# Performance work log

Hardware: AMD Instinct MI355X
Metric: run time of the kernel (lower is better)

The kernel has to match this reference:

```python
import jax, jax.numpy as jnp
import numpy as np

POS_SCALE = 50.0
LEN_SCALE = 500.0

N_NODES = 100000
N_EDGES = 600000
IN_DIM = 128
HID_DIM = 128


def setup_inputs() -> dict:
    key = jax.random.key(0)
    ks = jax.random.split(key, 12)
    x = jax.random.normal(ks[0], (N_NODES, IN_DIM), dtype=jnp.float32)
    positions = jax.random.randint(ks[1], (N_NODES,), 0, 50, dtype=jnp.int64)
    lengths = jax.random.randint(ks[2], (N_NODES,), 0, 500, dtype=jnp.int64)
    edge_index = jax.random.randint(ks[3], (2, N_EDGES), 0, N_NODES, dtype=jnp.int64)
    reranker_scores = jax.random.normal(ks[4], (N_NODES,), dtype=jnp.float32)
    s = 1.0 / np.sqrt(IN_DIM + 2)
    fp_w = jax.random.uniform(ks[5], (IN_DIM + 2, IN_DIM), minval=-s, maxval=s, dtype=jnp.float32)
    fp_b = jnp.zeros((IN_DIM,), jnp.float32)
    s2 = 1.0 / np.sqrt(IN_DIM)
    lin_l_w = jax.random.uniform(ks[6], (IN_DIM, HID_DIM), minval=-s2, maxval=s2, dtype=jnp.float32)
    lin_l_b = jnp.zeros((HID_DIM,), jnp.float32)
    lin_r_w = jax.random.uniform(ks[7], (IN_DIM, HID_DIM), minval=-s2, maxval=s2, dtype=jnp.float32)
    res_w = jax.random.uniform(ks[8], (IN_DIM, HID_DIM), minval=-s2, maxval=s2, dtype=jnp.float32)
    res_b = jnp.zeros((HID_DIM,), jnp.float32)
    s3 = 1.0 / np.sqrt(HID_DIM)
    sh_w = jax.random.uniform(ks[9], (HID_DIM, 1), minval=-s3, maxval=s3, dtype=jnp.float32)
    sh_b = jnp.zeros((1,), jnp.float32)
    alpha = jnp.asarray(0.65, jnp.float32)
    return {
        "x": x, "positions": positions, "lengths": lengths,
        "edge_index": edge_index, "reranker_scores": reranker_scores,
        "fp_w": fp_w, "fp_b": fp_b,
        "lin_l_w": lin_l_w, "lin_l_b": lin_l_b, "lin_r_w": lin_r_w,
        "res_w": res_w, "res_b": res_b,
        "sh_w": sh_w, "sh_b": sh_b, "alpha": alpha,
    }


def reference(x, positions, lengths, edge_index, reranker_scores,
              fp_w, fp_b, lin_l_w, lin_l_b, lin_r_w, res_w, res_b,
              sh_w, sh_b, alpha):
    n = x.shape[0]
    # position/length features
    pos_feat = positions[:, None].astype(x.dtype) / POS_SCALE
    len_feat = lengths[:, None].astype(x.dtype) / LEN_SCALE
    xf = jnp.concatenate([x, pos_feat, len_feat], axis=-1)  # [N, D+2]
    xf = xf @ fp_w + fp_b                                   # [N, D]
    h_in = xf @ res_w + res_b                               # residual proj [N, H]
    # SAGEConv with mean aggregation: out = lin_l(mean_{j->i} x_j) + lin_r(x_i)
    src, dst = edge_index[0], edge_index[1]
    msg_sum = jax.ops.segment_sum(xf[src], dst, num_segments=n)          # [N, D]
    cnt = jax.ops.segment_sum(jnp.ones((src.shape[0], 1), xf.dtype), dst, num_segments=n)
    agg = msg_sum / jnp.maximum(cnt, 1.0)
    h = jax.nn.relu(agg @ lin_l_w + lin_l_b + xf @ lin_r_w)  # [N, H]
    # dropout is identity in eval mode
    h = h + h_in
    gnn_scores = (h @ sh_w + sh_b)[:, 0]                     # [N]
    a = jax.nn.sigmoid(alpha)
    return a * reranker_scores + (1.0 - a) * gnn_scores
```

## Files before the change

### kernel.cpp

```cpp
#include <hip/hip_runtime.h>
#include <hip/hip_bf16.h>
#include <cstdint>

#define D 128
#define LDSPITCH 136
#define CAP 32

typedef __attribute__((ext_vector_type(4))) float f32x4;
typedef __attribute__((ext_vector_type(2))) float f32x2;
typedef __attribute__((ext_vector_type(8))) short s16x8;

__device__ __forceinline__ unsigned short f2b(float f) {
    union { float f; uint32_t u; } v; v.f = f;
    uint32_t b = v.u + 0x7fffu + ((v.u >> 16) & 1u);
    return (unsigned short)(b >> 16);
}
__device__ __forceinline__ float b2f(unsigned short u) {
    union { uint32_t u; float f; } v; v.u = ((uint32_t)u) << 16; return v.f;
}

#if __has_builtin(__builtin_amdgcn_cvt_pk_fp8_f32) && __has_builtin(__builtin_amdgcn_cvt_pk_f32_fp8)
#define FP8_HW 1
__device__ __forceinline__ unsigned char f_to_fp8(float f) {
    int r = __builtin_amdgcn_cvt_pk_fp8_f32(f, 0.f, 0, false);
    return (unsigned char)(r & 0xff);
}
__device__ __forceinline__ void fp8x8_acc(float* t, int wx, int wy) {
    f32x2 p0 = __builtin_amdgcn_cvt_pk_f32_fp8(wx, false);
    f32x2 p1 = __builtin_amdgcn_cvt_pk_f32_fp8(wx, true);
    f32x2 p2 = __builtin_amdgcn_cvt_pk_f32_fp8(wy, false);
    f32x2 p3 = __builtin_amdgcn_cvt_pk_f32_fp8(wy, true);
    t[0] += p0.x; t[1] += p0.y; t[2] += p1.x; t[3] += p1.y;
    t[4] += p2.x; t[5] += p2.y; t[6] += p3.x; t[7] += p3.y;
}
#else
__device__ __forceinline__ unsigned char f_to_fp8(float f) {
    union { float f; uint32_t u; } v; v.f = f;
    uint32_t s = (v.u >> 31) << 7;
    uint32_t bits = v.u & 0x7fffffffu;
    if (bits < 0x3a800000u) return (unsigned char)s;
    uint32_t r = bits + 0x7ffffu + ((bits >> 20) & 1u);
    int ee = (int)(r >> 23) - 127 + 7;
    uint32_t man = (r >> 20) & 7u;
    if (ee <= 0) return (unsigned char)s;
    if (ee > 15) { ee = 15; man = 6; }
    if (ee == 15 && man == 7) man = 6;
    return (unsigned char)(s | ((uint32_t)ee << 3) | man);
}
__device__ __forceinline__ float fp8_one(unsigned char u) {
    int s = u >> 7, e = (u >> 3) & 15, m = u & 7;
    if (e == 0) { float v = (float)m * 0.001953125f; return s ? -v : v; }
    union { uint32_t u; float f; } w;
    w.u = ((uint32_t)s << 31) | ((uint32_t)(e + 120) << 23) | ((uint32_t)m << 20);
    return w.f;
}
__device__ __forceinline__ void fp8x8_acc(float* t, int wx, int wy) {
    uint32_t a = (uint32_t)wx, b = (uint32_t)wy;
#pragma unroll
    for (int k = 0; k < 4; ++k) t[k] += fp8_one((a >> (8 * k)) & 0xff);
#pragma unroll
    for (int k = 0; k < 4; ++k) t[4 + k] += fp8_one((b >> (8 * k)) & 0xff);
}
#endif

__global__ __launch_bounds__(256) void k_prep(
    const float* __restrict__ fp_w, const float* __restrict__ lin_l_w,
    const float* __restrict__ lin_r_w,
    unsigned short* __restrict__ Btf, unsigned short* __restrict__ Btl,
    unsigned short* __restrict__ Btr,
    const float* __restrict__ res_w, const float* __restrict__ res_b,
    const float* __restrict__ sh_w, const float* __restrict__ sh_b,
    const float* __restrict__ alpha, float* __restrict__ c1, float* __restrict__ scal,
    int* __restrict__ cursor, int* __restrict__ srcs,
    unsigned short* __restrict__ xb, unsigned char* __restrict__ xf8,
    int N, int zb) {
    int bid = blockIdx.x, tid = threadIdx.x;
    if (bid < 192) {
        int m = bid >> 6;
        int i = (bid & 63) * 256 + tid;
        const float* src = (m == 0) ? fp_w : (m == 1) ? lin_l_w : lin_r_w;
        unsigned short* dst = (m == 0) ? Btf : (m == 1) ? Btl : Btr;
        int k = i >> 7, n = i & 127;
        dst[n * D + k] = f2b(src[k * D + n]);
    } else if (bid == 192) {
        if (tid < 128) {
            float s = 0.f;
            for (int j = 0; j < D; ++j) s += res_w[tid * D + j] * sh_w[j];
            c1[tid] = s;
            if (tid == 0) {
                float c0 = 0.f;
                for (int j = 0; j < D; ++j) c0 += res_b[j] * sh_w[j];
                c0 += sh_b[0];
                float a = 1.f / (1.f + expf(-alpha[0]));
                scal[0] = a; scal[1] = c0;
            }
        } else if (tid < 192) {
            ((unsigned int*)(xb + (size_t)N * D))[tid - 128] = 0u;
        } else if (tid < 224) {
            ((unsigned int*)(xf8 + (size_t)N * D))[tid - 192] = 0u;
        }
    } else if (bid < 193 + zb) {
        int i = ((bid - 193) * 256 + tid) * 4;
        if (i < N) {
            if (i + 3 < N) *(int4*)(cursor + i) = (int4){0, 0, 0, 0};
            else { for (int k = i; k < N; ++k) cursor[k] = 0; }
        }
    } else {
        int i = ((bid - 193 - zb) * 256 + tid) * 4;
        if (i < N * CAP) *(int4*)(srcs + i) = (int4){N, N, N, N};
    }
}

__global__ __launch_bounds__(256) void k_gemm1(
    const float* __restrict__ x, unsigned short* __restrict__ xb,
    unsigned char* __restrict__ xf8,
    const int* __restrict__ positions, const int* __restrict__ lengths,
    const unsigned short* __restrict__ Btf,
    const float* __restrict__ fp_w, const float* __restrict__ fp_b,
    const float* __restrict__ c1, float* __restrict__ d1, int N, int mb,
    const int* __restrict__ ei, int* __restrict__ cursor, int* __restrict__ srcs, int E) {
    if (blockIdx.x >= mb) {
        int e = (blockIdx.x - mb) * 256 + threadIdx.x;
        if (e < E) {
            int src = ei[e];
            int dst = ei[E + e];
            int pos = atomicAdd(&cursor[dst], 1);
            if (pos < CAP) srcs[dst * CAP + pos] = src;
        }
        return;
    }
    int lane = threadIdx.x & 63;
    int wv = threadIdx.x >> 6;
    int col = lane & 15, q = lane >> 4;
    int row0 = blockIdx.x * 64 + wv * 16;
    int arow = row0 + col; if (arow > N - 1) arow = N - 1;

    f32x4 acc[8];
#pragma unroll
    for (int nt = 0; nt < 8; ++nt) acc[nt] = (f32x4){0.f, 0.f, 0.f, 0.f};

#pragma unroll
    for (int ks = 0; ks < 4; ++ks) {
        const float* xp = x + (size_t)arow * D + ks * 32 + q * 8;
        float4 a0 = *(const float4*)xp;
        float4 a1 = *(const float4*)(xp + 4);
        s16x8 af;
        af[0] = (short)f2b(a0.x); af[1] = (short)f2b(a0.y);
        af[2] = (short)f2b(a0.z); af[3] = (short)f2b(a0.w);
        af[4] = (short)f2b(a1.x); af[5] = (short)f2b(a1.y);
        af[6] = (short)f2b(a1.z); af[7] = (short)f2b(a1.w);
#pragma unroll
        for (int nt = 0; nt < 8; ++nt) {
            s16x8 bf = *(const s16x8*)(Btf + (size_t)(nt * 16 + col) * D + ks * 32 + q * 8);
            acc[nt] = __builtin_amdgcn_mfma_f32_16x16x32_bf16(af, bf, acc[nt], 0, 0, 0);
        }
    }

    float pf[4], lf[4];
#pragma unroll
    for (int r = 0; r < 4; ++r) {
        int rr = row0 + q * 4 + r; int rc = rr < N ? rr : N - 1;
        pf[r] = (float)positions[rc] * (1.0f / 50.0f);
        lf[r] = (float)lengths[rc] * (1.0f / 500.0f);
    }
    float sdot[4] = {0.f, 0.f, 0.f, 0.f};
#pragma unroll
    for (int nt = 0; nt < 8; ++nt) {
        int n = nt * 16 + col;
        float bias = fp_b[n];
        float w128 = fp_w[128 * D + n];
        float w129 = fp_w[129 * D + n];
        float c1v = c1[n];
#pragma unroll
        for (int r = 0; r < 4; ++r) {
            float t = acc[nt][r] + bias + pf[r] * w128 + lf[r] * w129;
            int rr = row0 + q * 4 + r;
            if (rr < N) {
                xb[(size_t)rr * D + n] = f2b(t);
                xf8[(size_t)rr * D + n] = f_to_fp8(t);
            }
            sdot[r] += t * c1v;
        }
    }
#pragma unroll
    for (int r = 0; r < 4; ++r) {
        float s = sdot[r];
        s += __shfl_xor(s, 1, 64);
        s += __shfl_xor(s, 2, 64);
        s += __shfl_xor(s, 4, 64);
        s += __shfl_xor(s, 8, 64);
        if (col == 0) {
            int rr = row0 + q * 4 + r;
            if (rr < N) d1[rr] = s;
        }
    }
}

__global__ __launch_bounds__(256) void k_gemm2(
    const unsigned short* __restrict__ xfb, const unsigned char* __restrict__ xf8,
    const int* __restrict__ cursor, const int* __restrict__ srcs,
    const unsigned short* __restrict__ Btl, const unsigned short* __restrict__ Btr,
    const float* __restrict__ lin_l_b, const float* __restrict__ sh_w,
    const float* __restrict__ rer, const float* __restrict__ d1,
    const float* __restrict__ scal, float* __restrict__ out, int N) {
    __shared__ unsigned short agg[64 * LDSPITCH];
    int lane = threadIdx.x & 63;
    int wv = threadIdx.x >> 6;
    int li = lane & 15, q = lane >> 4;
    int wrow0 = blockIdx.x * 64 + wv * 16;

    int degs[4];
    const int* sp[4];
#pragma unroll
    for (int rr = 0; rr < 4; ++rr) {
        int row = wrow0 + rr * 4 + q;
        int ok = row < N;
        int dg = ok ? cursor[row] : 0;
        degs[rr] = dg > CAP ? CAP : dg;
        sp[rr] = srcs + (size_t)(ok ? row : 0) * CAP;
    }
    int dmax = degs[0] > degs[1] ? degs[0] : degs[1];
    if (degs[2] > dmax) dmax = degs[2];
    if (degs[3] > dmax) dmax = degs[3];
    dmax = max(dmax, __shfl_xor(dmax, 16, 64));
    dmax = max(dmax, __shfl_xor(dmax, 32, 64));
    int rounds = (dmax + 7) >> 3;

    float t[4][8];
#pragma unroll
    for (int rr = 0; rr < 4; ++rr)
#pragma unroll
        for (int k2 = 0; k2 < 8; ++k2) t[rr][k2] = 0.f;

    for (int jr = 0; jr < rounds; ++jr) {
        int j = jr * 8;
#pragma unroll
        for (int rr = 0; rr < 4; ++rr) {
            int4 ia = *(const int4*)(sp[rr] + j);
            int4 ib = *(const int4*)(sp[rr] + j + 4);
            int2 v0 = *(const int2*)(xf8 + (size_t)ia.x * D + li * 8);
            int2 v1 = *(const int2*)(xf8 + (size_t)ia.y * D + li * 8);
            int2 v2 = *(const int2*)(xf8 + (size_t)ia.z * D + li * 8);
            int2 v3 = *(const int2*)(xf8 + (size_t)ia.w * D + li * 8);
            int2 v4 = *(const int2*)(xf8 + (size_t)ib.x * D + li * 8);
            int2 v5 = *(const int2*)(xf8 + (size_t)ib.y * D + li * 8);
            int2 v6 = *(const int2*)(xf8 + (size_t)ib.z * D + li * 8);
            int2 v7 = *(const int2*)(xf8 + (size_t)ib.w * D + li * 8);
            fp8x8_acc(t[rr], v0.x, v0.y);
            fp8x8_acc(t[rr], v1.x, v1.y);
            fp8x8_acc(t[rr], v2.x, v2.y);
            fp8x8_acc(t[rr], v3.x, v3.y);
            fp8x8_acc(t[rr], v4.x, v4.y);
            fp8x8_acc(t[rr], v5.x, v5.y);
            fp8x8_acc(t[rr], v6.x, v6.y);
            fp8x8_acc(t[rr], v7.x, v7.y);
        }
    }

#pragma unroll
    for (int rr = 0; rr < 4; ++rr) {
        float rc = 1.0f / (float)(degs[rr] > 0 ? degs[rr] : 1);
        s16x8 o;
#pragma unroll
        for (int k2 = 0; k2 < 8; ++k2) o[k2] = (short)f2b(t[rr][k2] * rc);
        *(s16x8*)(agg + (wv * 16 + rr * 4 + q) * LDSPITCH + li * 8) = o;
    }

    int arow = wrow0 + li; if (arow > N - 1) arow = N - 1;

    f32x4 acc[8];
#pragma unroll
    for (int nt = 0; nt < 8; ++nt) acc[nt] = (f32x4){0.f, 0.f, 0.f, 0.f};

#pragma unroll
    for (int ks = 0; ks < 4; ++ks) {
        s16x8 af = *(const s16x8*)(agg + (wv * 16 + li) * LDSPITCH + ks * 32 + q * 8);
#pragma unroll
        for (int nt = 0; nt < 8; ++nt) {
            s16x8 bf = *(const s16x8*)(Btl + (size_t)(nt * 16 + li) * D + ks * 32 + q * 8);
            acc[nt] = __builtin_amdgcn_mfma_f32_16x16x32_bf16(af, bf, acc[nt], 0, 0, 0);
        }
    }
#pragma unroll
    for (int ks = 0; ks < 4; ++ks) {
        s16x8 af = *(const s16x8*)(xfb + (size_t)arow * D + ks * 32 + q * 8);
#pragma unroll
        for (int nt = 0; nt < 8; ++nt) {
            s16x8 bf = *(const s16x8*)(Btr + (size_t)(nt * 16 + li) * D + ks * 32 + q * 8);
            acc[nt] = __builtin_amdgcn_mfma_f32_16x16x32_bf16(af, bf, acc[nt], 0, 0, 0);
        }
    }

    float a = scal[0], c0 = scal[1];
    float sdot[4] = {0.f, 0.f, 0.f, 0.f};
#pragma unroll
    for (int nt = 0; nt < 8; ++nt) {
        int n = nt * 16 + li;
        float bias = lin_l_b[n];
        float shw = sh_w[n];
#pragma unroll
        for (int r = 0; r < 4; ++r) {
            float t2 = acc[nt][r] + bias;
            sdot[r] += fmaxf(t2, 0.f) * shw;
        }
    }
#pragma unroll
    for (int r = 0; r < 4; ++r) {
        float s = sdot[r];
        s += __shfl_xor(s, 1, 64);
        s += __shfl_xor(s, 2, 64);
        s += __shfl_xor(s, 4, 64);
        s += __shfl_xor(s, 8, 64);
        if (li == 0) {
            int rr = wrow0 + q * 4 + r;
            if (rr < N) out[rr] = a * rer[rr] + (1.f - a) * (c0 + d1[rr] + s);
        }
    }
}

extern "C" void kernel_launch(void* const* d_in, const int* in_sizes, int n_in,
                              void* d_out, int out_size, void* d_ws, size_t ws_size,
                              hipStream_t stream) {
    const float* x        = (const float*)d_in[0];
    const int*   positions= (const int*)d_in[1];
    const int*   lengths  = (const int*)d_in[2];
    const int*   ei       = (const int*)d_in[3];
    const float* rer      = (const float*)d_in[4];
    const float* fp_w     = (const float*)d_in[5];
    const float* fp_b     = (const float*)d_in[6];
    const float* lin_l_w  = (const float*)d_in[7];
    const float* lin_l_b  = (const float*)d_in[8];
    const float* lin_r_w  = (const float*)d_in[9];
    const float* res_w    = (const float*)d_in[10];
    const float* res_b    = (const float*)d_in[11];
    const float* sh_w     = (const float*)d_in[12];
    const float* sh_b     = (const float*)d_in[13];
    const float* alpha    = (const float*)d_in[14];
    int N = in_sizes[1];
    int E = in_sizes[3] / 2;
    float* out = (float*)d_out;

    char* ws = (char*)d_ws;
    size_t off = 0;
    auto alloc = [&](size_t bytes) -> void* {
        void* p = ws + off;
        off = (off + bytes + 255) & ~(size_t)255;
        return p;
    };
    unsigned short* xb  = (unsigned short*)alloc((size_t)(N + 1) * D * 2);
    unsigned char*  xf8 = (unsigned char*)alloc((size_t)(N + 1) * D);
    int* srcs    = (int*)alloc((size_t)N * CAP * 4);
    int* cursor  = (int*)alloc((size_t)N * 4);
    float* d1    = (float*)alloc((size_t)N * 4);
    unsigned short* Btf = (unsigned short*)alloc(D * D * 2);
    unsigned short* Btl = (unsigned short*)alloc(D * D * 2);
    unsigned short* Btr = (unsigned short*)alloc(D * D * 2);
    float* c1    = (float*)alloc(D * 4);
    float* scal  = (float*)alloc(16);

    int mb = (N + 63) / 64;
    int cb = (E + 255) / 256;
    int zb = (N + 1023) / 1024;
    int sb = (N * CAP / 4 + 255) / 256;

    k_prep<<<193 + zb + sb, 256, 0, stream>>>(fp_w, lin_l_w, lin_r_w, Btf, Btl, Btr,
                                              res_w, res_b, sh_w, sh_b, alpha, c1, scal,
                                              cursor, srcs, xb, xf8, N, zb);
    k_gemm1<<<mb + cb, 256, 0, stream>>>(x, xb, xf8, positions, lengths, Btf, fp_w, fp_b,
                                         c1, d1, N, mb, ei, cursor, srcs, E);
    k_gemm2<<<mb, 256, 0, stream>>>(xb, xf8, cursor, srcs, Btl, Btr, lin_l_b, sh_w,
                                    rer, d1, scal, out, N);
}
```

Baseline: 251.0 us.

## Split neighbor gather out of second GEMM into separate kernel

Moves the fp8 neighbor mean aggregation out of the fused gemm2 kernel into a standalone gather kernel. The new kernel assigns 8 lanes per row with 16-byte loads, and writes the bf16 aggregate to a global buffer that a simplified MFMA kernel then reads. The aim is better gather parallelism and occupancy, since the fused kernel's LDS use and MFMA register pressure no longer limit the gather. In exchange it adds an extra launch and a round trip to global memory for the aggregate, about 25MB written and read back.

```diff
diff --git a/kernel.cpp b/kernel.cpp
--- a/kernel.cpp
+++ b/kernel.cpp
@@ -3,7 +3,6 @@
 #include <cstdint>
 
 #define D 128
-#define LDSPITCH 136
 #define CAP 32
 
 typedef __attribute__((ext_vector_type(4))) float f32x4;
@@ -20,7 +19,6 @@
 }
 
 #if __has_builtin(__builtin_amdgcn_cvt_pk_fp8_f32) && __has_builtin(__builtin_amdgcn_cvt_pk_f32_fp8)
-#define FP8_HW 1
 __device__ __forceinline__ unsigned char f_to_fp8(float f) {
     int r = __builtin_amdgcn_cvt_pk_fp8_f32(f, 0.f, 0, false);
     return (unsigned char)(r & 0xff);
@@ -72,7 +70,7 @@
     const float* __restrict__ sh_w, const float* __restrict__ sh_b,
     const float* __restrict__ alpha, float* __restrict__ c1, float* __restrict__ scal,
     int* __restrict__ cursor, int* __restrict__ srcs,
-    unsigned short* __restrict__ xb, unsigned char* __restrict__ xf8,
+    unsigned char* __restrict__ xf8,
     int N, int zb) {
     int bid = blockIdx.x, tid = threadIdx.x;
     if (bid < 192) {
@@ -94,10 +92,8 @@
                 float a = 1.f / (1.f + expf(-alpha[0]));
                 scal[0] = a; scal[1] = c0;
             }
-        } else if (tid < 192) {
-            ((unsigned int*)(xb + (size_t)N * D))[tid - 128] = 0u;
-        } else if (tid < 224) {
-            ((unsigned int*)(xf8 + (size_t)N * D))[tid - 192] = 0u;
+        } else if (tid < 160) {
+            ((unsigned int*)(xf8 + (size_t)N * D))[tid - 128] = 0u;
         }
     } else if (bid < 193 + zb) {
         int i = ((bid - 193) * 256 + tid) * 4;
@@ -196,76 +192,75 @@
     }
 }
 
-__global__ __launch_bounds__(256) void k_gemm2(
-    const unsigned short* __restrict__ xfb, const unsigned char* __restrict__ xf8,
+__global__ __launch_bounds__(256) void k_gather(
+    const unsigned char* __restrict__ xf8,
     const int* __restrict__ cursor, const int* __restrict__ srcs,
+    unsigned short* __restrict__ aggb, int N) {
+    int lane = threadIdx.x & 63;
+    int wv = threadIdx.x >> 6;
+    int oct = lane >> 3, ol = lane & 7;
+    int row = (blockIdx.x * 4 + wv) * 8 + oct;
+    int ok = row < N;
+    int rowc = ok ? row : 0;
+    int deg = ok ? cursor[rowc] : 0;
+    if (deg > CAP) deg = CAP;
+    const int* sp = srcs + (size_t)rowc * CAP;
+
+    int dmax = deg;
+    dmax = max(dmax, __shfl_xor(dmax, 8, 64));
+    dmax = max(dmax, __shfl_xor(dmax, 16, 64));
+    dmax = max(dmax, __shfl_xor(dmax, 32, 64));
+    int rounds = (dmax + 7) >> 3;
+
+    float t[16];
+#pragma unroll
+    for (int k = 0; k < 16; ++k) t[k] = 0.f;
+
+    for (int jr = 0; jr < rounds; ++jr) {
+        int j = jr * 8;
+        int4 ia = *(const int4*)(sp + j);
+        int4 ib = *(const int4*)(sp + j + 4);
+        int4 v0 = *(const int4*)(xf8 + (size_t)ia.x * D + ol * 16);
+        int4 v1 = *(const int4*)(xf8 + (size_t)ia.y * D + ol * 16);
+        int4 v2 = *(const int4*)(xf8 + (size_t)ia.z * D + ol * 16);
+        int4 v3 = *(const int4*)(xf8 + (size_t)ia.w * D + ol * 16);
+        int4 v4 = *(const int4*)(xf8 + (size_t)ib.x * D + ol * 16);
+        int4 v5 = *(const int4*)(xf8 + (size_t)ib.y * D + ol * 16);
+        int4 v6 = *(const int4*)(xf8 + (size_t)ib.z * D + ol * 16);
+        int4 v7 = *(const int4*)(xf8 + (size_t)ib.w * D + ol * 16);
+        fp8x8_acc(t,     v0.x, v0.y); fp8x8_acc(t + 8, v0.z, v0.w);
+        fp8x8_acc(t,     v1.x, v1.y); fp8x8_acc(t + 8, v1.z, v1.w);
+        fp8x8_acc(t,     v2.x, v2.y); fp8x8_acc(t + 8, v2.z, v2.w);
+        fp8x8_acc(t,     v3.x, v3.y); fp8x8_acc(t + 8, v3.z, v3.w);
+        fp8x8_acc(t,     v4.x, v4.y); fp8x8_acc(t + 8, v4.z, v4.w);
+        fp8x8_acc(t,     v5.x, v5.y); fp8x8_acc(t + 8, v5.z, v5.w);
+        fp8x8_acc(t,     v6.x, v6.y); fp8x8_acc(t + 8, v6.z, v6.w);
+        fp8x8_acc(t,     v7.x, v7.y); fp8x8_acc(t + 8, v7.z, v7.w);
+    }
+
+    if (ok) {
+        float rc = 1.0f / (float)(deg > 0 ? deg : 1);
+        s16x8 o0, o1;
+#pragma unroll
+        for (int k = 0; k < 8; ++k) o0[k] = (short)f2b(t[k] * rc);
+#pragma unroll
+        for (int k = 0; k < 8; ++k) o1[k] = (short)f2b(t[8 + k] * rc);
+        unsigned short* dst = aggb + (size_t)row * D + ol * 16;
+        *(s16x8*)dst = o0;
+        *(s16x8*)(dst + 8) = o1;
+    }
+}
+
+__global__ __launch_bounds__(256) void k_gemm2d(
+    const unsigned short* __restrict__ xfb, const unsigned short* __restrict__ aggb,
     const unsigned short* __restrict__ Btl, const unsigned short* __restrict__ Btr,
     const float* __restrict__ lin_l_b, const float* __restrict__ sh_w,
     const float* __restrict__ rer, const float* __restrict__ d1,
     const float* __restrict__ scal, float* __restrict__ out, int N) {
-    __shared__ unsigned short agg[64 * LDSPITCH];
     int lane = threadIdx.x & 63;
     int wv = threadIdx.x >> 6;
     int li = lane & 15, q = lane >> 4;
     int wrow0 = blockIdx.x * 64 + wv * 16;
-
-    int degs[4];
-    const int* sp[4];
-#pragma unroll
-    for (int rr = 0; rr < 4; ++rr) {
-        int row = wrow0 + rr * 4 + q;
-        int ok = row < N;
-        int dg = ok ? cursor[row] : 0;
-        degs[rr] = dg > CAP ? CAP : dg;
-        sp[rr] = srcs + (size_t)(ok ? row : 0) * CAP;
-    }
-    int dmax = degs[0] > degs[1] ? degs[0] : degs[1];
-    if (degs[2] > dmax) dmax = degs[2];
-    if (degs[3] > dmax) dmax = degs[3];
-    dmax = max(dmax, __shfl_xor(dmax, 16, 64));
-    dmax = max(dmax, __shfl_xor(dmax, 32, 64));
-    int rounds = (dmax + 7) >> 3;
-
-    float t[4][8];
-#pragma unroll
-    for (int rr = 0; rr < 4; ++rr)
-#pragma unroll
-        for (int k2 = 0; k2 < 8; ++k2) t[rr][k2] = 0.f;
-
-    for (int jr = 0; jr < rounds; ++jr) {
-        int j = jr * 8;
-#pragma unroll
-        for (int rr = 0; rr < 4; ++rr) {
-            int4 ia = *(const int4*)(sp[rr] + j);
-            int4 ib = *(const int4*)(sp[rr] + j + 4);
-            int2 v0 = *(const int2*)(xf8 + (size_t)ia.x * D + li * 8);
-            int2 v1 = *(const int2*)(xf8 + (size_t)ia.y * D + li * 8);
-            int2 v2 = *(const int2*)(xf8 + (size_t)ia.z * D + li * 8);
-            int2 v3 = *(const int2*)(xf8 + (size_t)ia.w * D + li * 8);
-            int2 v4 = *(const int2*)(xf8 + (size_t)ib.x * D + li * 8);
-            int2 v5 = *(const int2*)(xf8 + (size_t)ib.y * D + li * 8);
-            int2 v6 = *(const int2*)(xf8 + (size_t)ib.z * D + li * 8);
-            int2 v7 = *(const int2*)(xf8 + (size_t)ib.w * D + li * 8);
-            fp8x8_acc(t[rr], v0.x, v0.y);
-            fp8x8_acc(t[rr], v1.x, v1.y);
-            fp8x8_acc(t[rr], v2.x, v2.y);
-            fp8x8_acc(t[rr], v3.x, v3.y);
-            fp8x8_acc(t[rr], v4.x, v4.y);
-            fp8x8_acc(t[rr], v5.x, v5.y);
-            fp8x8_acc(t[rr], v6.x, v6.y);
-            fp8x8_acc(t[rr], v7.x, v7.y);
-        }
-    }
-
-#pragma unroll
-    for (int rr = 0; rr < 4; ++rr) {
-        float rc = 1.0f / (float)(degs[rr] > 0 ? degs[rr] : 1);
-        s16x8 o;
-#pragma unroll
-        for (int k2 = 0; k2 < 8; ++k2) o[k2] = (short)f2b(t[rr][k2] * rc);
-        *(s16x8*)(agg + (wv * 16 + rr * 4 + q) * LDSPITCH + li * 8) = o;
-    }
-
     int arow = wrow0 + li; if (arow > N - 1) arow = N - 1;
 
     f32x4 acc[8];
@@ -274,7 +269,7 @@
 
 #pragma unroll
     for (int ks = 0; ks < 4; ++ks) {
-        s16x8 af = *(const s16x8*)(agg + (wv * 16 + li) * LDSPITCH + ks * 32 + q * 8);
+        s16x8 af = *(const s16x8*)(aggb + (size_t)arow * D + ks * 32 + q * 8);
 #pragma unroll
         for (int nt = 0; nt < 8; ++nt) {
             s16x8 bf = *(const s16x8*)(Btl + (size_t)(nt * 16 + li) * D + ks * 32 + q * 8);
@@ -347,8 +342,9 @@
         off = (off + bytes + 255) & ~(size_t)255;
         return p;
     };
-    unsigned short* xb  = (unsigned short*)alloc((size_t)(N + 1) * D * 2);
-    unsigned char*  xf8 = (unsigned char*)alloc((size_t)(N + 1) * D);
+    unsigned short* xb   = (unsigned short*)alloc((size_t)N * D * 2);
+    unsigned char*  xf8  = (unsigned char*)alloc((size_t)(N + 1) * D);
+    unsigned short* aggb = (unsigned short*)alloc((size_t)N * D * 2);
     int* srcs    = (int*)alloc((size_t)N * CAP * 4);
     int* cursor  = (int*)alloc((size_t)N * 4);
     float* d1    = (float*)alloc((size_t)N * 4);
@@ -362,12 +358,13 @@
     int cb = (E + 255) / 256;
     int zb = (N + 1023) / 1024;
     int sb = (N * CAP / 4 + 255) / 256;
+    int gb = (N + 31) / 32;
 
     k_prep<<<193 + zb + sb, 256, 0, stream>>>(fp_w, lin_l_w, lin_r_w, Btf, Btl, Btr,
                                               res_w, res_b, sh_w, sh_b, alpha, c1, scal,
-                                              cursor, srcs, xb, xf8, N, zb);
+                                              cursor, srcs, xf8, N, zb);
     k_gemm1<<<mb + cb, 256, 0, stream>>>(x, xb, xf8, positions, lengths, Btf, fp_w, fp_b,
                                          c1, d1, N, mb, ei, cursor, srcs, E);
-    k_gemm2<<<mb, 256, 0, stream>>>(xb, xf8, cursor, srcs, Btl, Btr, lin_l_b, sh_w,
-                                    rer, d1, scal, out, N);
-}
+    k_gather<<<gb, 256, 0, stream>>>(xf8, cursor, srcs, aggb, N);
+    k_gemm2d<<<mb, 256, 0, stream>>>(xb, aggb, Btl, Btr, lin_l_b, sh_w, rer, d1, scal, out, N);
+}
```

After: 262.3 us. +4.5%, slower.

## Drop bf16 feature copy, transpose neighbor list, broadcast indices via shuffles

Applied to the files above, without the earlier changes.

Removes the bf16 copy of the projected features and feeds the root-term MFMA from the fp8 copy, converting fp8 to bf16 in registers. This cuts one N×128×2-byte write and a later read. The neighbor-index table is stored slot-major (pos*N+dst) so each lane loads one slot for a row, and indices are handed out with wave shuffles instead of vector loads per row. The cost is extra shuffles and conversion ALU work, plus lower precision on the lin_r input, which is now fp8 instead of bf16.

```diff
diff --git a/kernel.cpp b/kernel.cpp
--- a/kernel.cpp
+++ b/kernel.cpp
@@ -15,23 +15,19 @@
     uint32_t b = v.u + 0x7fffu + ((v.u >> 16) & 1u);
     return (unsigned short)(b >> 16);
 }
-__device__ __forceinline__ float b2f(unsigned short u) {
-    union { uint32_t u; float f; } v; v.u = ((uint32_t)u) << 16; return v.f;
-}
 
 #if __has_builtin(__builtin_amdgcn_cvt_pk_fp8_f32) && __has_builtin(__builtin_amdgcn_cvt_pk_f32_fp8)
-#define FP8_HW 1
 __device__ __forceinline__ unsigned char f_to_fp8(float f) {
     int r = __builtin_amdgcn_cvt_pk_fp8_f32(f, 0.f, 0, false);
     return (unsigned char)(r & 0xff);
 }
-__device__ __forceinline__ void fp8x8_acc(float* t, int wx, int wy) {
+__device__ __forceinline__ void fp8x8_to_f32(float* o, int wx, int wy) {
     f32x2 p0 = __builtin_amdgcn_cvt_pk_f32_fp8(wx, false);
     f32x2 p1 = __builtin_amdgcn_cvt_pk_f32_fp8(wx, true);
     f32x2 p2 = __builtin_amdgcn_cvt_pk_f32_fp8(wy, false);
     f32x2 p3 = __builtin_amdgcn_cvt_pk_f32_fp8(wy, true);
-    t[0] += p0.x; t[1] += p0.y; t[2] += p1.x; t[3] += p1.y;
-    t[4] += p2.x; t[5] += p2.y; t[6] += p3.x; t[7] += p3.y;
+    o[0] = p0.x; o[1] = p0.y; o[2] = p1.x; o[3] = p1.y;
+    o[4] = p2.x; o[5] = p2.y; o[6] = p3.x; o[7] = p3.y;
 }
 #else
 __device__ __forceinline__ unsigned char f_to_fp8(float f) {
@@ -54,14 +50,20 @@
     w.u = ((uint32_t)s << 31) | ((uint32_t)(e + 120) << 23) | ((uint32_t)m << 20);
     return w.f;
 }
+__device__ __forceinline__ void fp8x8_to_f32(float* o, int wx, int wy) {
+    uint32_t a = (uint32_t)wx, b = (uint32_t)wy;
+#pragma unroll
+    for (int k = 0; k < 4; ++k) o[k] = fp8_one((a >> (8 * k)) & 0xff);
+#pragma unroll
+    for (int k = 0; k < 4; ++k) o[4 + k] = fp8_one((b >> (8 * k)) & 0xff);
+}
+#endif
 __device__ __forceinline__ void fp8x8_acc(float* t, int wx, int wy) {
-    uint32_t a = (uint32_t)wx, b = (uint32_t)wy;
-#pragma unroll
-    for (int k = 0; k < 4; ++k) t[k] += fp8_one((a >> (8 * k)) & 0xff);
-#pragma unroll
-    for (int k = 0; k < 4; ++k) t[4 + k] += fp8_one((b >> (8 * k)) & 0xff);
-}
-#endif
+    float o[8];
+    fp8x8_to_f32(o, wx, wy);
+#pragma unroll
+    for (int k = 0; k < 8; ++k) t[k] += o[k];
+}
 
 __global__ __launch_bounds__(256) void k_prep(
     const float* __restrict__ fp_w, const float* __restrict__ lin_l_w,
@@ -72,8 +74,7 @@
     const float* __restrict__ sh_w, const float* __restrict__ sh_b,
     const float* __restrict__ alpha, float* __restrict__ c1, float* __restrict__ scal,
     int* __restrict__ cursor, int* __restrict__ srcs,
-    unsigned short* __restrict__ xb, unsigned char* __restrict__ xf8,
-    int N, int zb) {
+    unsigned char* __restrict__ xf8, int N, int zb) {
     int bid = blockIdx.x, tid = threadIdx.x;
     if (bid < 192) {
         int m = bid >> 6;
@@ -94,10 +95,8 @@
                 float a = 1.f / (1.f + expf(-alpha[0]));
                 scal[0] = a; scal[1] = c0;
             }
-        } else if (tid < 192) {
-            ((unsigned int*)(xb + (size_t)N * D))[tid - 128] = 0u;
-        } else if (tid < 224) {
-            ((unsigned int*)(xf8 + (size_t)N * D))[tid - 192] = 0u;
+        } else if (tid < 160) {
+            ((unsigned int*)(xf8 + (size_t)N * D))[tid - 128] = 0u;
         }
     } else if (bid < 193 + zb) {
         int i = ((bid - 193) * 256 + tid) * 4;
@@ -112,8 +111,7 @@
 }
 
 __global__ __launch_bounds__(256) void k_gemm1(
-    const float* __restrict__ x, unsigned short* __restrict__ xb,
-    unsigned char* __restrict__ xf8,
+    const float* __restrict__ x, unsigned char* __restrict__ xf8,
     const int* __restrict__ positions, const int* __restrict__ lengths,
     const unsigned short* __restrict__ Btf,
     const float* __restrict__ fp_w, const float* __restrict__ fp_b,
@@ -125,7 +123,7 @@
             int src = ei[e];
             int dst = ei[E + e];
             int pos = atomicAdd(&cursor[dst], 1);
-            if (pos < CAP) srcs[dst * CAP + pos] = src;
+            if (pos < CAP) srcs[(size_t)pos * N + dst] = src;
         }
         return;
     }
@@ -175,10 +173,7 @@
         for (int r = 0; r < 4; ++r) {
             float t = acc[nt][r] + bias + pf[r] * w128 + lf[r] * w129;
             int rr = row0 + q * 4 + r;
-            if (rr < N) {
-                xb[(size_t)rr * D + n] = f2b(t);
-                xf8[(size_t)rr * D + n] = f_to_fp8(t);
-            }
+            if (rr < N) xf8[(size_t)rr * D + n] = f_to_fp8(t);
             sdot[r] += t * c1v;
         }
     }
@@ -197,7 +192,7 @@
 }
 
 __global__ __launch_bounds__(256) void k_gemm2(
-    const unsigned short* __restrict__ xfb, const unsigned char* __restrict__ xf8,
+    const unsigned char* __restrict__ xf8,
     const int* __restrict__ cursor, const int* __restrict__ srcs,
     const unsigned short* __restrict__ Btl, const unsigned short* __restrict__ Btr,
     const float* __restrict__ lin_l_b, const float* __restrict__ sh_w,
@@ -209,19 +204,19 @@
     int li = lane & 15, q = lane >> 4;
     int wrow0 = blockIdx.x * 64 + wv * 16;
 
-    int degs[4];
-    const int* sp[4];
+    int idxA[4], idxB[4], degs[4];
+    int dmax = 0;
 #pragma unroll
     for (int rr = 0; rr < 4; ++rr) {
         int row = wrow0 + rr * 4 + q;
         int ok = row < N;
-        int dg = ok ? cursor[row] : 0;
-        degs[rr] = dg > CAP ? CAP : dg;
-        sp[rr] = srcs + (size_t)(ok ? row : 0) * CAP;
-    }
-    int dmax = degs[0] > degs[1] ? degs[0] : degs[1];
-    if (degs[2] > dmax) dmax = degs[2];
-    if (degs[3] > dmax) dmax = degs[3];
+        int dg = ok ? cursor[ok ? row : 0] : 0;
+        if (dg > CAP) dg = CAP;
+        degs[rr] = dg;
+        if (dg > dmax) dmax = dg;
+        idxA[rr] = ok ? srcs[(size_t)li * N + row] : N;
+        idxB[rr] = ok ? srcs[(size_t)(16 + li) * N + row] : N;
+    }
     dmax = max(dmax, __shfl_xor(dmax, 16, 64));
     dmax = max(dmax, __shfl_xor(dmax, 32, 64));
     int rounds = (dmax + 7) >> 3;
@@ -232,20 +227,28 @@
 #pragma unroll
         for (int k2 = 0; k2 < 8; ++k2) t[rr][k2] = 0.f;
 
+    int qbase = lane & 48;
     for (int jr = 0; jr < rounds; ++jr) {
-        int j = jr * 8;
+        int lo = qbase + ((jr & 1) << 3);
 #pragma unroll
         for (int rr = 0; rr < 4; ++rr) {
-            int4 ia = *(const int4*)(sp[rr] + j);
-            int4 ib = *(const int4*)(sp[rr] + j + 4);
-            int2 v0 = *(const int2*)(xf8 + (size_t)ia.x * D + li * 8);
-            int2 v1 = *(const int2*)(xf8 + (size_t)ia.y * D + li * 8);
-            int2 v2 = *(const int2*)(xf8 + (size_t)ia.z * D + li * 8);
-            int2 v3 = *(const int2*)(xf8 + (size_t)ia.w * D + li * 8);
-            int2 v4 = *(const int2*)(xf8 + (size_t)ib.x * D + li * 8);
-            int2 v5 = *(const int2*)(xf8 + (size_t)ib.y * D + li * 8);
-            int2 v6 = *(const int2*)(xf8 + (size_t)ib.z * D + li * 8);
-            int2 v7 = *(const int2*)(xf8 + (size_t)ib.w * D + li * 8);
+            int sel = (jr & 2) ? idxB[rr] : idxA[rr];
+            int i0 = __shfl(sel, lo + 0, 64);
+            int i1 = __shfl(sel, lo + 1, 64);
+            int i2 = __shfl(sel, lo + 2, 64);
+            int i3 = __shfl(sel, lo + 3, 64);
+            int i4 = __shfl(sel, lo + 4, 64);
+            int i5 = __shfl(sel, lo + 5, 64);
+            int i6 = __shfl(sel, lo + 6, 64);
+            int i7 = __shfl(sel, lo + 7, 64);
+            int2 v0 = *(const int2*)(xf8 + (size_t)i0 * D + li * 8);
+            int2 v1 = *(const int2*)(xf8 + (size_t)i1 * D + li * 8);
+            int2 v2 = *(const int2*)(xf8 + (size_t)i2 * D + li * 8);
+            int2 v3 = *(const int2*)(xf8 + (size_t)i3 * D + li * 8);
+            int2 v4 = *(const int2*)(xf8 + (size_t)i4 * D + li * 8);
+            int2 v5 = *(const int2*)(xf8 + (size_t)i5 * D + li * 8);
+            int2 v6 = *(const int2*)(xf8 + (size_t)i6 * D + li * 8);
+            int2 v7 = *(const int2*)(xf8 + (size_t)i7 * D + li * 8);
             fp8x8_acc(t[rr], v0.x, v0.y);
             fp8x8_acc(t[rr], v1.x, v1.y);
             fp8x8_acc(t[rr], v2.x, v2.y);
@@ -283,7 +286,12 @@
     }
 #pragma unroll
     for (int ks = 0; ks < 4; ++ks) {
-        s16x8 af = *(const s16x8*)(xfb + (size_t)arow * D + ks * 32 + q * 8);
+        int2 raw = *(const int2*)(xf8 + (size_t)arow * D + ks * 32 + q * 8);
+        float o[8];
+        fp8x8_to_f32(o, raw.x, raw.y);
+        s16x8 af;
+#pragma unroll
+        for (int k2 = 0; k2 < 8; ++k2) af[k2] = (short)f2b(o[k2]);
 #pragma unroll
         for (int nt = 0; nt < 8; ++nt) {
             s16x8 bf = *(const s16x8*)(Btr + (size_t)(nt * 16 + li) * D + ks * 32 + q * 8);
@@ -347,7 +355,6 @@
         off = (off + bytes + 255) & ~(size_t)255;
         return p;
     };
-    unsigned short* xb  = (unsigned short*)alloc((size_t)(N + 1) * D * 2);
     unsigned char*  xf8 = (unsigned char*)alloc((size_t)(N + 1) * D);
     int* srcs    = (int*)alloc((size_t)N * CAP * 4);
     int* cursor  = (int*)alloc((size_t)N * 4);
@@ -365,9 +372,9 @@
 
     k_prep<<<193 + zb + sb, 256, 0, stream>>>(fp_w, lin_l_w, lin_r_w, Btf, Btl, Btr,
                                               res_w, res_b, sh_w, sh_b, alpha, c1, scal,
-                                              cursor, srcs, xb, xf8, N, zb);
-    k_gemm1<<<mb + cb, 256, 0, stream>>>(x, xb, xf8, positions, lengths, Btf, fp_w, fp_b,
+                                              cursor, srcs, xf8, N, zb);
+    k_gemm1<<<mb + cb, 256, 0, stream>>>(x, xf8, positions, lengths, Btf, fp_w, fp_b,
                                          c1, d1, N, mb, ei, cursor, srcs, E);
-    k_gemm2<<<mb, 256, 0, stream>>>(xb, xf8, cursor, srcs, Btl, Btr, lin_l_b, sh_w,
+    k_gemm2<<<mb, 256, 0, stream>>>(xf8, cursor, srcs, Btl, Btr, lin_l_b, sh_w,
                                     rer, d1, scal, out, N);
 }
```

Measured after the change: 260.8 us. 1.04x slower.
